# Kernel tuning notes

Measured on AMD Instinct MI355X. Metric: run time of the kernel, lower is better.

The kernel has to match this reference:

```python
import jax, jax.numpy as jnp
import numpy as np

N_XI = 512      # internal REN state dim
L = 128         # nonlinearity channels (sequential loop length)
N_STATES = 128  # plant state dim (w)
N_INPUTS = 64   # control input dim (u)
EPS = 0.001
STD = 0.1
BATCH = 32768


def _model_params(X, Y):
    """set_model_param(): derive constrained REN matrices from free params X, Y."""
    n, l = N_XI, L
    H = X.T @ X + EPS * jnp.eye(2 * n + l, dtype=X.dtype)
    H11 = H[:n, :n]
    H21 = H[n:n + l, :n]
    H22 = H[n:n + l, n:n + l]
    H31 = H[n + l:, :n]
    H32 = H[n + l:, n:n + l]
    H33 = H[n + l:, n + l:]
    Fm = H31                                 # (n_xi, n_xi)
    B1 = H32                                 # (n_xi, l)
    E = 0.5 * (H11 + H33 + Y - Y.T)          # (n_xi, n_xi)
    Lam = 0.5 * jnp.diag(H22)                # (l,) strictly positive
    D11 = -jnp.tril(H22, -1)                 # strictly lower triangular (l, l)
    C1 = -H21                                # (l, n_xi)
    return Fm, B1, E, Lam, D11, C1


def setup_inputs() -> dict:
    key = jax.random.key(0)
    ks = jax.random.split(key, 9)
    n, l = N_XI, L
    return {
        "t": 0,
        "w": jax.random.normal(ks[0], (BATCH, 1, N_STATES), jnp.float32),
        "xi": jax.random.normal(ks[1], (BATCH, 1, n), jnp.float32),
        "X": jax.random.normal(ks[2], (2 * n + l, 2 * n + l), jnp.float32) * STD,
        "Y": jax.random.normal(ks[3], (n, n), jnp.float32) * STD,
        "B2": jax.random.normal(ks[4], (n, N_STATES), jnp.float32) * STD,
        "C2": jax.random.normal(ks[5], (N_INPUTS, n), jnp.float32) * STD,
        "D21": jax.random.normal(ks[6], (N_INPUTS, l), jnp.float32) * STD,
        "D22": jax.random.normal(ks[7], (N_INPUTS, N_STATES), jnp.float32) * STD,
        "D12": jax.random.normal(ks[8], (l, N_STATES), jnp.float32) * STD,
    }


def reference(t, w, xi, X, Y, B2, C2, D21, D22, D12):
    Fm, B1, E, Lam, D11, C1 = _model_params(X, Y)
    w2 = w[:, 0, :]    # (B, num_states)
    xi2 = xi[:, 0, :]  # (B, n_xi)

    # Precompute the xi- and w-dependent parts of every row's pre-activation.
    pre = xi2 @ C1.T + w2 @ D12.T  # (B, l)

    eye = jnp.eye(L, dtype=pre.dtype)

    def step(eps, xs):
        # Sequential forward substitution: row i only reads eps[:, :i]
        # because D11 is strictly lower triangular.
        d_row, p_col, lam, e_row = xs
        v = p_col + eps @ d_row            # (B,)
        e = jnp.tanh(v / lam)
        return eps + e[:, None] * e_row[None, :], None

    eps0 = jnp.zeros_like(pre)
    epsilon, _ = jax.lax.scan(step, eps0, (D11, pre.T, Lam, eye))  # (B, l)

    E_xi = xi2 @ Fm.T + epsilon @ B1.T + w2 @ B2.T      # (B, n_xi)
    xi_ = E_xi @ jnp.linalg.inv(E).T                    # (B, n_xi)
    u = xi2 @ C2.T + epsilon @ D21.T + w2 @ D22.T       # (B, num_inputs)
    return u[:, None, :], xi_[:, None, :]
```

## Files before the change

kernel.cpp:

```cpp
#include <hip/hip_runtime.h>
#include <cstddef>

#define NXI   512
#define LL    128
#define NST   128
#define NU    64
#define BATCH 32768
#define TW    1152
#define EPSC  0.001f
#define KC    768
#define NC    576
#define NCP   640
#define GJB   133

typedef unsigned short u16;
typedef __attribute__((ext_vector_type(8))) short   short8;
typedef __attribute__((ext_vector_type(4))) short   short4v;
typedef __attribute__((ext_vector_type(4))) float   f32x4;

__device__ __forceinline__ u16 f2bf(float f) {
    unsigned u = __float_as_uint(f);
    u += 0x7FFFu + ((u >> 16) & 1u);
    return (u16)(u >> 16);
}

__device__ __forceinline__ void gbar(int* cnt, int* gen, int nblk) {
    __syncthreads();
    if (threadIdx.x == 0) {
        int g = __hip_atomic_load(gen, __ATOMIC_RELAXED, __HIP_MEMORY_SCOPE_AGENT);
        if (__hip_atomic_fetch_add(cnt, 1, __ATOMIC_RELEASE, __HIP_MEMORY_SCOPE_AGENT) == nblk - 1) {
            __hip_atomic_store(cnt, 0, __ATOMIC_RELAXED, __HIP_MEMORY_SCOPE_AGENT);
            __hip_atomic_fetch_add(gen, 1, __ATOMIC_RELEASE, __HIP_MEMORY_SCOPE_AGENT);
        } else {
            int spins = 0;
            while (__hip_atomic_load(gen, __ATOMIC_RELAXED, __HIP_MEMORY_SCOPE_AGENT) == g) {
                __builtin_amdgcn_s_sleep(8);
                if (++spins > (1 << 20)) break;
            }
        }
        (void)__hip_atomic_load(gen, __ATOMIC_ACQUIRE, __HIP_MEMORY_SCOPE_AGENT);
    }
    __syncthreads();
}

__global__ __launch_bounds__(256) void k_setup(const float* __restrict__ X, u16* __restrict__ XT,
                                               const float* __restrict__ xi, const float* __restrict__ w,
                                               u16* __restrict__ Ac, int* __restrict__ bar) {
    __shared__ float t[32][33];
    int blk = blockIdx.x;
    if (blk < 1296) {
        if (blk == 0 && threadIdx.x < 2) bar[threadIdx.x] = 0;
        int tx = threadIdx.x & 31, ty = threadIdx.x >> 5;
        int bx = blk % 36, by = blk / 36;
        #pragma unroll
        for (int q = 0; q < 4; q++) {
            int r = ty + q * 8;
            t[r][tx] = X[(size_t)(by * 32 + r) * TW + bx * 32 + tx];
        }
        __syncthreads();
        #pragma unroll
        for (int q = 0; q < 4; q++) {
            int r = ty + q * 8;
            XT[(size_t)(bx * 32 + r) * TW + by * 32 + tx] = f2bf(t[tx][r]);
        }
        return;
    }
    size_t tt = (size_t)(blk - 1296) * 256 + threadIdx.x;
    int b = (int)(tt / 80), ch = (int)(tt % 80);
    const float* src;
    int col;
    if (ch < 64) { src = xi + (size_t)b * NXI + ch * 8;        col = ch * 8; }
    else         { src = w  + (size_t)b * NST + (ch - 64) * 8; col = 640 + (ch - 64) * 8; }
    f32x4 a = ((const f32x4*)src)[0], c = ((const f32x4*)src)[1];
    short8 o;
    o[0]=(short)f2bf(a[0]); o[1]=(short)f2bf(a[1]); o[2]=(short)f2bf(a[2]); o[3]=(short)f2bf(a[3]);
    o[4]=(short)f2bf(c[0]); o[5]=(short)f2bf(c[1]); o[6]=(short)f2bf(c[2]); o[7]=(short)f2bf(c[3]);
    *(short8*)(Ac + (size_t)b * KC + col) = o;
}

__global__ __launch_bounds__(256) void k_gemm2(const u16* __restrict__ A, int lda,
                                               const u16* __restrict__ W, int ldw,
                                               float* __restrict__ C0, int ldc0, int nsplit,
                                               float* __restrict__ C1, int ldc1,
                                               int K, int nbx, int ntrue, int swz) {
    __shared__ __align__(16) u16 As[2][128 * 32];
    __shared__ __align__(16) u16 Bs[2][128 * 32];
    int id = blockIdx.x;
    int bx, by;
    if (swz) {
        int j = id >> 3;
        int per = (int)(gridDim.x >> 3) / nbx;
        by = (id & 7) * per + j / nbx;
        bx = j - (j / nbx) * nbx;
    } else {
        by = id / nbx;
        bx = id - by * nbx;
    }
    const int tid = threadIdx.x;
    const int wave = tid >> 6, lane = tid & 63, quad = lane >> 4, l16 = lane & 15;
    const int bm0 = by * 128, bn0 = bx * 128;
    const int srow = tid >> 2;
    const int sch = (((tid & 3) ^ ((srow >> 2) & 3))) * 8;
    const u16* ga0 = A + (size_t)(bm0 + srow) * lda + sch;
    const u16* ga1 = ga0 + (size_t)64 * lda;
    const u16* gb0 = W + (size_t)(bn0 + srow) * ldw + sch;
    const u16* gb1 = gb0 + (size_t)64 * ldw;
    const int lo = wave * 512;
    const int mb = (wave >> 1) * 64, nb = (wave & 1) * 64;
    const int rch = (quad ^ (l16 >> 2)) * 8;

    f32x4 acc[4][4];
    #pragma unroll
    for (int i = 0; i < 4; i++)
        #pragma unroll
        for (int j = 0; j < 4; j++) acc[i][j] = (f32x4){0.f, 0.f, 0.f, 0.f};

    const int nk = K >> 5;
    __builtin_amdgcn_global_load_lds((void*)(ga0), (void*)(As[0] + lo),        16, 0, 0);
    __builtin_amdgcn_global_load_lds((void*)(ga1), (void*)(As[0] + lo + 2048), 16, 0, 0);
    __builtin_amdgcn_global_load_lds((void*)(gb0), (void*)(Bs[0] + lo),        16, 0, 0);
    __builtin_amdgcn_global_load_lds((void*)(gb1), (void*)(Bs[0] + lo + 2048), 16, 0, 0);
    __syncthreads();
    int cur = 0;
    for (int t = 0; t < nk; ++t) {
        if (t + 1 < nk) {
            const int kt = (t + 1) << 5;
            const int nx = cur ^ 1;
            __builtin_amdgcn_global_load_lds((void*)(ga0 + kt), (void*)(As[nx] + lo),        16, 0, 0);
            __builtin_amdgcn_global_load_lds((void*)(ga1 + kt), (void*)(As[nx] + lo + 2048), 16, 0, 0);
            __builtin_amdgcn_global_load_lds((void*)(gb0 + kt), (void*)(Bs[nx] + lo),        16, 0, 0);
            __builtin_amdgcn_global_load_lds((void*)(gb1 + kt), (void*)(Bs[nx] + lo + 2048), 16, 0, 0);
        }
        const u16* as = As[cur];
        const u16* bs = Bs[cur];
        short8 af[4], bf[4];
        #pragma unroll
        for (int mt = 0; mt < 4; mt++) af[mt] = *(const short8*)&as[(mb + mt * 16 + l16) * 32 + rch];
        #pragma unroll
        for (int nt = 0; nt < 4; nt++) bf[nt] = *(const short8*)&bs[(nb + nt * 16 + l16) * 32 + rch];
        #pragma unroll
        for (int mt = 0; mt < 4; mt++)
            #pragma unroll
            for (int nt = 0; nt < 4; nt++)
                acc[mt][nt] = __builtin_amdgcn_mfma_f32_16x16x32_bf16(af[mt], bf[nt], acc[mt][nt], 0, 0, 0);
        __syncthreads();
        cur ^= 1;
    }
    #pragma unroll
    for (int mt = 0; mt < 4; mt++)
        #pragma unroll
        for (int nt = 0; nt < 4; nt++)
            #pragma unroll
            for (int r = 0; r < 4; r++) {
                int row = bm0 + mb + mt * 16 + quad * 4 + r;
                int col = bn0 + nb + nt * 16 + l16;
                if (col < ntrue) {
                    float v = acc[mt][nt][r];
                    if (col < nsplit) C0[(size_t)row * ldc0 + col] = v;
                    else              C1[(size_t)row * ldc1 + (col - nsplit)] = v;
                }
            }
}

__global__ __launch_bounds__(256) void k_derive(const float* __restrict__ Hm, const float* __restrict__ Y,
                                                const float* __restrict__ B2, const float* __restrict__ D12,
                                                float* __restrict__ Agj, float* __restrict__ D11,
                                                float* __restrict__ rlam, u16* __restrict__ W1) {
    int idx = blockIdx.x * 256 + threadIdx.x;
    const int n0 = 512 * 1280, n1 = 128 * 128, n2 = 128, n3 = 128 * KC;
    if (idx < n0) {
        int i = idx / 1280, j = idx % 1280;
        float val;
        if (j < 512) {
            val = 0.5f * (Hm[(size_t)i * TW + j] + Hm[(size_t)(640 + i) * TW + 640 + j]
                          + Y[(size_t)i * 512 + j] - Y[(size_t)j * 512 + i]);
            if (i == j) val += EPSC;
        } else if (j < 1024) {
            val = Hm[(size_t)(640 + i) * TW + (j - 512)];
        } else if (j < 1152) {
            val = Hm[(size_t)(640 + i) * TW + 512 + (j - 1024)];
        } else {
            val = B2[(size_t)i * NST + (j - 1152)];
        }
        Agj[idx] = val;
        return;
    }
    idx -= n0;
    if (idx < n1) {
        int i = idx >> 7, j = idx & 127;
        D11[idx] = (j < i) ? -Hm[(size_t)(512 + i) * TW + 512 + j] : 0.f;
        return;
    }
    idx -= n1;
    if (idx < n2) {
        rlam[idx] = 2.0f / (Hm[(size_t)(512 + idx) * TW + 512 + idx] + EPSC);
        return;
    }
    idx -= n2;
    if (idx < n3) {
        int i = idx / KC, c = idx % KC;
        float v;
        if (c < 512)      v = -Hm[(size_t)(512 + i) * TW + c];
        else if (c < 640) v = 0.f;
        else              v = D12[(size_t)i * NST + (c - 640)];
        W1[(size_t)i * KC + c] = f2bf(v);
    }
}

__device__ __forceinline__ void invert64(float* Cl, float* Sa, float* Sb, float* mcol,
                                         float* rp, float* __restrict__ invOut, int tid) {
    int r = tid >> 2, c = tid & 3;
    float a[16], b[16];
    #pragma unroll
    for (int q = 0; q < 4; q++) {
        f32x4 v = *(f32x4*)&Cl[r * 68 + c * 16 + q * 4];
        a[q*4+0]=v[0]; a[q*4+1]=v[1]; a[q*4+2]=v[2]; a[q*4+3]=v[3];
    }
    #pragma unroll
    for (int j = 0; j < 16; j++) b[j] = (c * 16 + j == r) ? 1.f : 0.f;

    #pragma unroll
    for (int k = 0; k < 64; k++) {
        const int p = (k & 1) << 6;
        const int kc = k >> 4, kl = k & 15;
        if (r == k) {
            #pragma unroll
            for (int q = 0; q < 4; q++) {
                *(f32x4*)&Sa[p + c * 16 + q * 4] = (f32x4){a[q*4], a[q*4+1], a[q*4+2], a[q*4+3]};
                *(f32x4*)&Sb[p + c * 16 + q * 4] = (f32x4){b[q*4], b[q*4+1], b[q*4+2], b[q*4+3]};
            }
        }
        if (c == kc) {
            mcol[p + r] = a[kl];
            if (r == k) rp[k & 1] = 1.0f / a[kl];
        }
        __syncthreads();
        float m = (mcol[p + r] - ((r == k) ? 1.0f : 0.0f)) * rp[k & 1];
        #pragma unroll
        for (int q = 0; q < 4; q++) {
            f32x4 sa = *(f32x4*)&Sa[p + c * 16 + q * 4];
            f32x4 sb = *(f32x4*)&Sb[p + c * 16 + q * 4];
            a[q*4+0] = fmaf(-m, sa[0], a[q*4+0]); a[q*4+1] = fmaf(-m, sa[1], a[q*4+1]);
            a[q*4+2] = fmaf(-m, sa[2], a[q*4+2]); a[q*4+3] = fmaf(-m, sa[3], a[q*4+3]);
            b[q*4+0] = fmaf(-m, sb[0], b[q*4+0]); b[q*4+1] = fmaf(-m, sb[1], b[q*4+1]);
            b[q*4+2] = fmaf(-m, sb[2], b[q*4+2]); b[q*4+3] = fmaf(-m, sb[3], b[q*4+3]);
        }
    }
    #pragma unroll
    for (int q = 0; q < 4; q++)
        *(f32x4*)&invOut[r * 64 + c * 16 + q * 4] = (f32x4){b[q*4], b[q*4+1], b[q*4+2], b[q*4+3]};
}

__global__ __launch_bounds__(256) void k_gj_fused(
        float* __restrict__ Agj, float* __restrict__ invD,
        const float* __restrict__ C2, const float* __restrict__ D21,
        const float* __restrict__ D22, u16* __restrict__ Wc,
        const u16* __restrict__ Ac, const u16* __restrict__ W1, float* __restrict__ pre,
        int* __restrict__ bar) {
    __shared__ __align__(16) float sm[4 * 4352 + 386];
    const int tid = threadIdx.x;
    const int id = blockIdx.x;

    if (id >= GJB) {
        u16* AsB = (u16*)sm;
        u16* BsB = (u16*)sm + 8192;
        const int by = id - GJB;
        const int wave = tid >> 6, lane = tid & 63, quad = lane >> 4, l16 = lane & 15;
        const int bm0 = by * 128;
        const int srow = tid >> 2;
        const int sch = (((tid & 3) ^ ((srow >> 2) & 3))) * 8;
        const u16* ga0 = Ac + (size_t)(bm0 + srow) * KC + sch;
        const u16* ga1 = ga0 + (size_t)64 * KC;
        const u16* gb0 = W1 + (size_t)srow * KC + sch;
        const u16* gb1 = gb0 + (size_t)64 * KC;
        const int lo = wave * 512;
        const int mb = (wave >> 1) * 64, nb = (wave & 1) * 64;
        const int rch = (quad ^ (l16 >> 2)) * 8;
        f32x4 acc[4][4];
        #pragma unroll
        for (int i = 0; i < 4; i++)
            #pragma unroll
            for (int j = 0; j < 4; j++) acc[i][j] = (f32x4){0.f, 0.f, 0.f, 0.f};
        __builtin_amdgcn_global_load_lds((void*)(ga0), (void*)(AsB + lo),        16, 0, 0);
        __builtin_amdgcn_global_load_lds((void*)(ga1), (void*)(AsB + lo + 2048), 16, 0, 0);
        __builtin_amdgcn_global_load_lds((void*)(gb0), (void*)(BsB + lo),        16, 0, 0);
        __builtin_amdgcn_global_load_lds((void*)(gb1), (void*)(BsB + lo + 2048), 16, 0, 0);
        __syncthreads();
        int cur = 0;
        for (int t = 0; t < 24; ++t) {
            if (t + 1 < 24) {
                const int kt = (t + 1) << 5;
                const int nx = cur ^ 1;
                __builtin_amdgcn_global_load_lds((void*)(ga0 + kt), (void*)(AsB + nx * 4096 + lo),        16, 0, 0);
                __builtin_amdgcn_global_load_lds((void*)(ga1 + kt), (void*)(AsB + nx * 4096 + lo + 2048), 16, 0, 0);
                __builtin_amdgcn_global_load_lds((void*)(gb0 + kt), (void*)(BsB + nx * 4096 + lo),        16, 0, 0);
                __builtin_amdgcn_global_load_lds((void*)(gb1 + kt), (void*)(BsB + nx * 4096 + lo + 2048), 16, 0, 0);
            }
            const u16* as = AsB + cur * 4096;
            const u16* bs = BsB + cur * 4096;
            short8 af[4], bf[4];
            #pragma unroll
            for (int mt = 0; mt < 4; mt++) af[mt] = *(const short8*)&as[(mb + mt * 16 + l16) * 32 + rch];
            #pragma unroll
            for (int nt = 0; nt < 4; nt++) bf[nt] = *(const short8*)&bs[(nb + nt * 16 + l16) * 32 + rch];
            #pragma unroll
            for (int mt = 0; mt < 4; mt++)
                #pragma unroll
                for (int nt = 0; nt < 4; nt++)
                    acc[mt][nt] = __builtin_amdgcn_mfma_f32_16x16x32_bf16(af[mt], bf[nt], acc[mt][nt], 0, 0, 0);
            __syncthreads();
            cur ^= 1;
        }
        #pragma unroll
        for (int mt = 0; mt < 4; mt++)
            #pragma unroll
            for (int nt = 0; nt < 4; nt++)
                #pragma unroll
                for (int r = 0; r < 4; r++)
                    pre[(size_t)(bm0 + mb + mt * 16 + quad * 4 + r) * LL + (nb + nt * 16 + l16)] = acc[mt][nt][r];
        return;
    }

    float* invDs = sm;
    float* Ps    = sm + 4352;
    float* Ss    = sm + 8704;
    float* Ms    = sm + 13056;
    float* Sa    = sm + 17408;
    float* Sb    = Sa + 128;
    float* mcol  = Sb + 128;
    float* rp    = mcol + 128;
    int* cnt = bar;
    int* gen = bar + 1;

    if (id == 0) {
        int r = tid >> 2, c4 = tid & 3;
        #pragma unroll
        for (int q = 0; q < 4; q++)
            *(f32x4*)&Ps[r * 68 + c4 * 16 + q * 4] = *(const f32x4*)(Agj + (size_t)r * 1280 + c4 * 16 + q * 4);
        __syncthreads();
        invert64(Ps, Sa, Sb, mcol, rp, invD, tid);
    }
    gbar(cnt, gen, GJB);

    for (int k = 0; k < 8; k++) {
        const int nbk = 7 * (19 - k);
        if (id < nbk) {
            const int by = id % 7, bx = id / 7;
            const int rb = by + (by >= k ? 1 : 0);
            const int cb = k + 1 + bx;
            int lr = tid >> 2, lc = tid & 3;
            #pragma unroll
            for (int q = 0; q < 4; q++) {
                *(f32x4*)&invDs[lr * 68 + lc * 16 + q * 4] = *(const f32x4*)(invD + (size_t)k * 4096 + lr * 64 + lc * 16 + q * 4);
                *(f32x4*)&Ps[lr * 68 + lc * 16 + q * 4]    = *(const f32x4*)(Agj + (size_t)(k * 64 + lr) * 1280 + cb * 64 + lc * 16 + q * 4);
                *(f32x4*)&Ms[lr * 68 + lc * 16 + q * 4]    = *(const f32x4*)(Agj + (size_t)(rb * 64 + lr) * 1280 + k * 64 + lc * 16 + q * 4);
            }
            __syncthreads();
            int ty = tid >> 4, tx = tid & 15;
            f32x4 s[4];
            #pragma unroll
            for (int ri = 0; ri < 4; ri++) s[ri] = (f32x4){0.f, 0.f, 0.f, 0.f};
            for (int kk = 0; kk < 64; kk++) {
                f32x4 pv = *(f32x4*)&Ps[kk * 68 + tx * 4];
                #pragma unroll
                for (int ri = 0; ri < 4; ri++) s[ri] += pv * invDs[(ty * 4 + ri) * 68 + kk];
            }
            #pragma unroll
            for (int ri = 0; ri < 4; ri++) *(f32x4*)&Ss[(ty * 4 + ri) * 68 + tx * 4] = s[ri];
            __syncthreads();
            f32x4 accv[4];
            #pragma unroll
            for (int ri = 0; ri < 4; ri++)
                accv[ri] = *(const f32x4*)(Agj + (size_t)(rb * 64 + ty * 4 + ri) * 1280 + cb * 64 + tx * 4);
            for (int kk = 0; kk < 64; kk++) {
                f32x4 sv = *(f32x4*)&Ss[kk * 68 + tx * 4];
                #pragma unroll
                for (int ri = 0; ri < 4; ri++) accv[ri] -= sv * Ms[(ty * 4 + ri) * 68 + kk];
            }
            #pragma unroll
            for (int ri = 0; ri < 4; ri++)
                *(f32x4*)(Agj + (size_t)(rb * 64 + ty * 4 + ri) * 1280 + cb * 64 + tx * 4) = accv[ri];
            if (k < 7 && bx == 0 && by == k) {
                __syncthreads();
                #pragma unroll
                for (int ri = 0; ri < 4; ri++) *(f32x4*)&Ps[(ty * 4 + ri) * 68 + tx * 4] = accv[ri];
                __syncthreads();
                invert64(Ps, Sa, Sb, mcol, rp, invD + (size_t)(k + 1) * 4096, tid);
            }
        }
        gbar(cnt, gen, GJB);
    }

    if (id < 120) {
        const int bx = id % 12, by = id / 12;
        int ty = tid >> 4, tx = tid & 15;
        if (by >= 8) {
            #pragma unroll
            for (int ri = 0; ri < 4; ri++) {
                int q = ty * 4 + ri;
                int row = 512 + (by - 8) * 64 + q;
                int cbase = bx * 64 + tx * 4;
                short4v o;
                if (by == 8) {
                    f32x4 v;
                    if (cbase < 512)      v = *(const f32x4*)(C2 + (size_t)q * 512 + cbase);
                    else if (cbase < 640) v = *(const f32x4*)(D21 + (size_t)q * NST + (cbase - 512));
                    else                  v = *(const f32x4*)(D22 + (size_t)q * NST + (cbase - 640));
                    o[0]=(short)f2bf(v[0]); o[1]=(short)f2bf(v[1]); o[2]=(short)f2bf(v[2]); o[3]=(short)f2bf(v[3]);
                } else {
                    o[0]=0; o[1]=0; o[2]=0; o[3]=0;
                }
                *(short4v*)(Wc + (size_t)row * KC + cbase) = o;
            }
            return;
        }
        int lr = tid >> 2, lc = tid & 3;
        #pragma unroll
        for (int q = 0; q < 4; q++) {
            *(f32x4*)&invDs[lr * 68 + lc * 16 + q * 4] = *(const f32x4*)(invD + (size_t)by * 4096 + lr * 64 + lc * 16 + q * 4);
            *(f32x4*)&Ps[lr * 68 + lc * 16 + q * 4]    = *(const f32x4*)(Agj + (size_t)(by * 64 + lr) * 1280 + 512 + bx * 64 + lc * 16 + q * 4);
        }
        __syncthreads();
        f32x4 s[4];
        #pragma unroll
        for (int ri = 0; ri < 4; ri++) s[ri] = (f32x4){0.f, 0.f, 0.f, 0.f};
        for (int kk = 0; kk < 64; kk++) {
            f32x4 pv = *(f32x4*)&Ps[kk * 68 + tx * 4];
            #pragma unroll
            for (int ri = 0; ri < 4; ri++) s[ri] += pv * invDs[(ty * 4 + ri) * 68 + kk];
        }
        #pragma unroll
        for (int ri = 0; ri < 4; ri++) {
            short4v o; o[0]=(short)f2bf(s[ri][0]); o[1]=(short)f2bf(s[ri][1]); o[2]=(short)f2bf(s[ri][2]); o[3]=(short)f2bf(s[ri][3]);
            *(short4v*)(Wc + (size_t)(by * 64 + ty * 4 + ri) * KC + bx * 64 + tx * 4) = o;
        }
    }
}

__global__ __launch_bounds__(1024) void k_scan(const float* __restrict__ pre, const float* __restrict__ D11,
                                               const float* __restrict__ rlam, u16* __restrict__ Ac) {
    __shared__ __align__(16) float D11s[128 * 132];
    int tid = threadIdx.x;
    {
        int r = tid >> 3, c = (tid & 7) * 16;
        const f32x4* src = (const f32x4*)(D11 + (size_t)r * 128 + c);
        f32x4 v0 = src[0], v1 = src[1], v2 = src[2], v3 = src[3];
        f32x4* dst = (f32x4*)&D11s[r * 132 + c];
        dst[0] = v0; dst[1] = v1; dst[2] = v2; dst[3] = v3;
    }
    int lg = tid & 15;
    int row = blockIdx.x * 64 + (tid >> 4);
    int gbase = (tid & 63) & ~15;
    const float L2E2 = 2.885390082f;

    float corrv[8], a8[8];
    #pragma unroll
    for (int b = 0; b < 8; b++) {
        corrv[b] = pre[(size_t)row * 128 + b * 16 + lg];
        a8[b] = L2E2 * rlam[b * 16 + lg];
    }
    __syncthreads();

    #pragma unroll
    for (int b = 0; b < 8; b++) {
        f32x4 dblk[4];
        #pragma unroll
        for (int q = 0; q < 4; q++)
            dblk[q] = *(const f32x4*)&D11s[(b * 16 + lg) * 132 + b * 16 + q * 4];
        float v = corrv[b];
        float a = a8[b];
        float e16[16];
        float myeps = 0.f;
        #pragma unroll
        for (int t = 0; t < 16; t++) {
            float ex = __builtin_amdgcn_exp2f(a * v);
            float cand = 1.0f - 2.0f * __builtin_amdgcn_rcpf(ex + 1.0f);
            float e = __shfl(cand, gbase + t, 64);
            e16[t] = e;
            if (lg == t) myeps = e;
            v = fmaf(e, dblk[t >> 2][t & 3], v);
        }
        Ac[(size_t)row * KC + 512 + b * 16 + lg] = f2bf(myeps);
        #pragma unroll
        for (int bb = b + 1; bb < 8; bb++) {
            f32x4 dd[4];
            #pragma unroll
            for (int q = 0; q < 4; q++)
                dd[q] = *(const f32x4*)&D11s[(bb * 16 + lg) * 132 + b * 16 + q * 4];
            float acc = corrv[bb];
            #pragma unroll
            for (int t = 0; t < 16; t++)
                acc = fmaf(e16[t], dd[t >> 2][t & 3], acc);
            corrv[bb] = acc;
        }
    }
}

extern "C" void kernel_launch(void* const* d_in, const int* in_sizes, int n_in,
                              void* d_out, int out_size, void* d_ws, size_t ws_size,
                              hipStream_t stream) {
    const float* w_in  = (const float*)d_in[1];
    const float* xi_in = (const float*)d_in[2];
    const float* X   = (const float*)d_in[3];
    const float* Y   = (const float*)d_in[4];
    const float* B2  = (const float*)d_in[5];
    const float* C2  = (const float*)d_in[6];
    const float* D21 = (const float*)d_in[7];
    const float* D22 = (const float*)d_in[8];
    const float* D12 = (const float*)d_in[9];
    float* out_u  = (float*)d_out;
    float* out_xi = (float*)d_out + (size_t)BATCH * NU;

    char* base = (char*)d_ws;
    size_t off = 0;
    auto carve = [&](size_t bytes) -> void* {
        void* p = base + off;
        off += (bytes + 255) & ~(size_t)255;
        return p;
    };
    u16*   XT   = (u16*)  carve((size_t)TW * TW * 2);
    u16*   Ac   = (u16*)  carve((size_t)BATCH * KC * 2);
    float* Hm   = (float*)carve((size_t)TW * TW * 4);
    float* Agj  = (float*)carve((size_t)512 * 1280 * 4);
    float* invD = (float*)carve((size_t)8 * 64 * 64 * 4);
    u16*   Wc   = (u16*)  carve((size_t)NCP * KC * 2);
    u16*   W1   = (u16*)  carve((size_t)LL * KC * 2);
    float* pre  = (float*)carve((size_t)BATCH * LL * 4);
    float* D11  = (float*)carve((size_t)LL * LL * 4);
    float* rlam = (float*)carve((size_t)LL * 4);
    int*   bar  = (int*)  carve(256);
    (void)ws_size; (void)in_sizes; (void)n_in; (void)out_size;

    k_setup<<<1296 + BATCH * 80 / 256, 256, 0, stream>>>(X, XT, xi_in, w_in, Ac, bar);
    k_gemm2<<<81, 256, 0, stream>>>(XT, TW, XT, TW, Hm, TW, 1 << 30, nullptr, 0, TW, 9, TW, 0);
    k_derive<<<(512 * 1280 + 128 * 128 + 128 + 128 * KC + 255) / 256, 256, 0, stream>>>(
        Hm, Y, B2, D12, Agj, D11, rlam, W1);
    k_gj_fused<<<GJB + 256, 256, 0, stream>>>(Agj, invD, C2, D21, D22, Wc, Ac, W1, pre, bar);
    k_scan<<<BATCH / 64, 1024, 0, stream>>>(pre, D11, rlam, Ac);
    k_gemm2<<<1280, 256, 0, stream>>>(Ac, KC, Wc, KC, out_xi, NXI, 512, out_u, NU, KC, 5, NC, 1);
}
```

Before: 544.4 us.

## Unfuse pre GEMM from Gauss-Jordan kernel and use single-wave 64x64 inversion

Moves the batch pre-activation GEMM out of the fused Gauss-Jordan kernel into its own k_gemm2 launch, so the GJ kernel now launches only its 133 cooperative blocks. It also replaces the 256-thread block-synchronized 64x64 diagonal inversion with an in-place single-wave Gauss-Jordan that needs no __syncthreads per pivot. The aim is to cut the barrier-heavy serial inversion latency on the critical path. In exchange, the GEMM no longer overlaps with the GJ phase and pays an extra launch, and the inversion runs on one wave with only one thread per row.

```diff
diff --git a/kernel.cpp b/kernel.cpp
--- a/kernel.cpp
+++ b/kernel.cpp
@@ -207,128 +207,45 @@
     }
 }
 
-__device__ __forceinline__ void invert64(float* Cl, float* Sa, float* Sb, float* mcol,
-                                         float* rp, float* __restrict__ invOut, int tid) {
-    int r = tid >> 2, c = tid & 3;
-    float a[16], b[16];
-    #pragma unroll
-    for (int q = 0; q < 4; q++) {
-        f32x4 v = *(f32x4*)&Cl[r * 68 + c * 16 + q * 4];
-        a[q*4+0]=v[0]; a[q*4+1]=v[1]; a[q*4+2]=v[2]; a[q*4+3]=v[3];
-    }
-    #pragma unroll
-    for (int j = 0; j < 16; j++) b[j] = (c * 16 + j == r) ? 1.f : 0.f;
-
-    #pragma unroll
-    for (int k = 0; k < 64; k++) {
-        const int p = (k & 1) << 6;
-        const int kc = k >> 4, kl = k & 15;
-        if (r == k) {
-            #pragma unroll
-            for (int q = 0; q < 4; q++) {
-                *(f32x4*)&Sa[p + c * 16 + q * 4] = (f32x4){a[q*4], a[q*4+1], a[q*4+2], a[q*4+3]};
-                *(f32x4*)&Sb[p + c * 16 + q * 4] = (f32x4){b[q*4], b[q*4+1], b[q*4+2], b[q*4+3]};
-            }
-        }
-        if (c == kc) {
-            mcol[p + r] = a[kl];
-            if (r == k) rp[k & 1] = 1.0f / a[kl];
-        }
-        __syncthreads();
-        float m = (mcol[p + r] - ((r == k) ? 1.0f : 0.0f)) * rp[k & 1];
-        #pragma unroll
-        for (int q = 0; q < 4; q++) {
-            f32x4 sa = *(f32x4*)&Sa[p + c * 16 + q * 4];
-            f32x4 sb = *(f32x4*)&Sb[p + c * 16 + q * 4];
-            a[q*4+0] = fmaf(-m, sa[0], a[q*4+0]); a[q*4+1] = fmaf(-m, sa[1], a[q*4+1]);
-            a[q*4+2] = fmaf(-m, sa[2], a[q*4+2]); a[q*4+3] = fmaf(-m, sa[3], a[q*4+3]);
-            b[q*4+0] = fmaf(-m, sb[0], b[q*4+0]); b[q*4+1] = fmaf(-m, sb[1], b[q*4+1]);
-            b[q*4+2] = fmaf(-m, sb[2], b[q*4+2]); b[q*4+3] = fmaf(-m, sb[3], b[q*4+3]);
-        }
-    }
-    #pragma unroll
-    for (int q = 0; q < 4; q++)
-        *(f32x4*)&invOut[r * 64 + c * 16 + q * 4] = (f32x4){b[q*4], b[q*4+1], b[q*4+2], b[q*4+3]};
+__device__ __forceinline__ void inv64_wave(float* rows, float* __restrict__ invOut, int tid) {
+    if (tid < 64) {
+        const int r = tid;
+        for (int k = 0; k < 64; ++k) {
+            float ip = 1.0f / rows[k * 68 + k];
+            f32x4 sr[16];
+            #pragma unroll
+            for (int c = 0; c < 16; ++c)
+                sr[c] = (*(const f32x4*)&rows[k * 68 + c * 4]) * ip;
+            float m = rows[r * 68 + k];
+            const bool piv = (r == k);
+            #pragma unroll
+            for (int c = 0; c < 16; ++c) {
+                f32x4 cur = *(const f32x4*)&rows[r * 68 + c * 4];
+                f32x4 nw = cur - m * sr[c];
+                if (piv) nw = sr[c];
+                *(f32x4*)&rows[r * 68 + c * 4] = nw;
+            }
+            rows[r * 68 + k] = piv ? ip : -m * ip;
+        }
+        #pragma unroll
+        for (int c = 0; c < 16; ++c)
+            *(f32x4*)&invOut[r * 64 + c * 4] = *(const f32x4*)&rows[r * 68 + c * 4];
+    }
 }
 
 __global__ __launch_bounds__(256) void k_gj_fused(
         float* __restrict__ Agj, float* __restrict__ invD,
         const float* __restrict__ C2, const float* __restrict__ D21,
         const float* __restrict__ D22, u16* __restrict__ Wc,
-        const u16* __restrict__ Ac, const u16* __restrict__ W1, float* __restrict__ pre,
         int* __restrict__ bar) {
-    __shared__ __align__(16) float sm[4 * 4352 + 386];
+    __shared__ __align__(16) float sm[4 * 4352];
     const int tid = threadIdx.x;
     const int id = blockIdx.x;
-
-    if (id >= GJB) {
-        u16* AsB = (u16*)sm;
-        u16* BsB = (u16*)sm + 8192;
-        const int by = id - GJB;
-        const int wave = tid >> 6, lane = tid & 63, quad = lane >> 4, l16 = lane & 15;
-        const int bm0 = by * 128;
-        const int srow = tid >> 2;
-        const int sch = (((tid & 3) ^ ((srow >> 2) & 3))) * 8;
-        const u16* ga0 = Ac + (size_t)(bm0 + srow) * KC + sch;
-        const u16* ga1 = ga0 + (size_t)64 * KC;
-        const u16* gb0 = W1 + (size_t)srow * KC + sch;
-        const u16* gb1 = gb0 + (size_t)64 * KC;
-        const int lo = wave * 512;
-        const int mb = (wave >> 1) * 64, nb = (wave & 1) * 64;
-        const int rch = (quad ^ (l16 >> 2)) * 8;
-        f32x4 acc[4][4];
-        #pragma unroll
-        for (int i = 0; i < 4; i++)
-            #pragma unroll
-            for (int j = 0; j < 4; j++) acc[i][j] = (f32x4){0.f, 0.f, 0.f, 0.f};
-        __builtin_amdgcn_global_load_lds((void*)(ga0), (void*)(AsB + lo),        16, 0, 0);
-        __builtin_amdgcn_global_load_lds((void*)(ga1), (void*)(AsB + lo + 2048), 16, 0, 0);
-        __builtin_amdgcn_global_load_lds((void*)(gb0), (void*)(BsB + lo),        16, 0, 0);
-        __builtin_amdgcn_global_load_lds((void*)(gb1), (void*)(BsB + lo + 2048), 16, 0, 0);
-        __syncthreads();
-        int cur = 0;
-        for (int t = 0; t < 24; ++t) {
-            if (t + 1 < 24) {
-                const int kt = (t + 1) << 5;
-                const int nx = cur ^ 1;
-                __builtin_amdgcn_global_load_lds((void*)(ga0 + kt), (void*)(AsB + nx * 4096 + lo),        16, 0, 0);
-                __builtin_amdgcn_global_load_lds((void*)(ga1 + kt), (void*)(AsB + nx * 4096 + lo + 2048), 16, 0, 0);
-                __builtin_amdgcn_global_load_lds((void*)(gb0 + kt), (void*)(BsB + nx * 4096 + lo),        16, 0, 0);
-                __builtin_amdgcn_global_load_lds((void*)(gb1 + kt), (void*)(BsB + nx * 4096 + lo + 2048), 16, 0, 0);
-            }
-            const u16* as = AsB + cur * 4096;
-            const u16* bs = BsB + cur * 4096;
-            short8 af[4], bf[4];
-            #pragma unroll
-            for (int mt = 0; mt < 4; mt++) af[mt] = *(const short8*)&as[(mb + mt * 16 + l16) * 32 + rch];
-            #pragma unroll
-            for (int nt = 0; nt < 4; nt++) bf[nt] = *(const short8*)&bs[(nb + nt * 16 + l16) * 32 + rch];
-            #pragma unroll
-            for (int mt = 0; mt < 4; mt++)
-                #pragma unroll
-                for (int nt = 0; nt < 4; nt++)
-                    acc[mt][nt] = __builtin_amdgcn_mfma_f32_16x16x32_bf16(af[mt], bf[nt], acc[mt][nt], 0, 0, 0);
-            __syncthreads();
-            cur ^= 1;
-        }
-        #pragma unroll
-        for (int mt = 0; mt < 4; mt++)
-            #pragma unroll
-            for (int nt = 0; nt < 4; nt++)
-                #pragma unroll
-                for (int r = 0; r < 4; r++)
-                    pre[(size_t)(bm0 + mb + mt * 16 + quad * 4 + r) * LL + (nb + nt * 16 + l16)] = acc[mt][nt][r];
-        return;
-    }
 
     float* invDs = sm;
     float* Ps    = sm + 4352;
     float* Ss    = sm + 8704;
     float* Ms    = sm + 13056;
-    float* Sa    = sm + 17408;
-    float* Sb    = Sa + 128;
-    float* mcol  = Sb + 128;
-    float* rp    = mcol + 128;
     int* cnt = bar;
     int* gen = bar + 1;
 
@@ -338,7 +255,7 @@
         for (int q = 0; q < 4; q++)
             *(f32x4*)&Ps[r * 68 + c4 * 16 + q * 4] = *(const f32x4*)(Agj + (size_t)r * 1280 + c4 * 16 + q * 4);
         __syncthreads();
-        invert64(Ps, Sa, Sb, mcol, rp, invD, tid);
+        inv64_wave(Ps, invD, tid);
     }
     gbar(cnt, gen, GJB);
 
@@ -385,7 +302,7 @@
                 #pragma unroll
                 for (int ri = 0; ri < 4; ri++) *(f32x4*)&Ps[(ty * 4 + ri) * 68 + tx * 4] = accv[ri];
                 __syncthreads();
-                invert64(Ps, Sa, Sb, mcol, rp, invD + (size_t)(k + 1) * 4096, tid);
+                inv64_wave(Ps, invD + (size_t)(k + 1) * 4096, tid);
             }
         }
         gbar(cnt, gen, GJB);
@@ -535,7 +452,8 @@
     k_gemm2<<<81, 256, 0, stream>>>(XT, TW, XT, TW, Hm, TW, 1 << 30, nullptr, 0, TW, 9, TW, 0);
     k_derive<<<(512 * 1280 + 128 * 128 + 128 + 128 * KC + 255) / 256, 256, 0, stream>>>(
         Hm, Y, B2, D12, Agj, D11, rlam, W1);
-    k_gj_fused<<<GJB + 256, 256, 0, stream>>>(Agj, invD, C2, D21, D22, Wc, Ac, W1, pre, bar);
+    k_gemm2<<<256, 256, 0, stream>>>(Ac, KC, W1, KC, pre, LL, 1 << 30, nullptr, 0, KC, 1, LL, 1);
+    k_gj_fused<<<GJB, 256, 0, stream>>>(Agj, invD, C2, D21, D22, Wc, bar);
     k_scan<<<BATCH / 64, 1024, 0, stream>>>(pre, D11, rlam, Ac);
     k_gemm2<<<1280, 256, 0, stream>>>(Ac, KC, Wc, KC, out_xi, NXI, 512, out_u, NU, KC, 5, NC, 1);
 }
```

Result: slower. 683.6 us (+25.6%).
